# Optimization experiments

Measured on AMD Instinct MI355X. Metric: run time of the kernel, lower is better.

The kernel has to match this reference:

```python
import jax, jax.numpy as jnp
import numpy as np

NUM_NODES = 65536       # B * gcn_nodes_num = 256 * 256
NODES_PER_GRAPH = 256
GCN_EMB_DIM = 128
N_EMBD = 512
NUM_EDGES = 1048576     # avg degree 16
NEG_SLOPE = 0.1


def gcn_conv(x, edge_index, W, b, num_nodes):
    """PyG GCNConv: add self-loops, symmetric normalization, linear, aggregate."""
    loop = jnp.arange(num_nodes, dtype=edge_index.dtype)
    src = jnp.concatenate([edge_index[0], loop])
    dst = jnp.concatenate([edge_index[1], loop])
    deg = jax.ops.segment_sum(jnp.ones_like(dst, dtype=x.dtype), dst,
                              num_segments=num_nodes)
    dinv = jnp.where(deg > 0, jax.lax.rsqrt(deg), jnp.zeros_like(deg))
    norm = dinv[src] * dinv[dst]              # [E+N]
    h = x @ W                                 # [N, out]
    msg = h[src] * norm[:, None]              # [E+N, out]
    out = jax.ops.segment_sum(msg, dst, num_segments=num_nodes)
    return out + b


def setup_inputs() -> dict:
    key = jax.random.key(0)
    ks = jax.random.split(key, 8)
    nodes = jax.random.normal(ks[0], (NUM_NODES, 3), dtype=jnp.float32)
    edge_index = jax.random.randint(ks[1], (2, NUM_EDGES), 0, NUM_NODES,
                                    dtype=jnp.int64)
    W1 = jax.random.normal(ks[2], (3, 3), dtype=jnp.float32) * 0.5
    b1 = jnp.zeros((3,), dtype=jnp.float32)
    W2 = jax.random.normal(ks[3], (3, GCN_EMB_DIM), dtype=jnp.float32) * 0.5
    b2 = jnp.zeros((GCN_EMB_DIM,), dtype=jnp.float32)
    W3 = jax.random.normal(ks[4], (GCN_EMB_DIM * NODES_PER_GRAPH, N_EMBD),
                           dtype=jnp.float32) * 0.01
    b3 = jnp.zeros((N_EMBD,), dtype=jnp.float32)
    return {"nodes": nodes, "edge_index": edge_index,
            "W1": W1, "b1": b1, "W2": W2, "b2": b2, "W3": W3, "b3": b3}


def reference(nodes, edge_index, W1, b1, W2, b2, W3, b3):
    n = nodes.shape[0]
    h = gcn_conv(nodes, edge_index, W1, b1, n)           # GCNConv(3,3)
    h = jnp.where(h >= 0, h, NEG_SLOPE * h)              # leaky_relu(0.1)
    h = gcn_conv(h, edge_index, W2, b2, n)               # GCNConv(3,128)
    h = h.reshape(-1, GCN_EMB_DIM * NODES_PER_GRAPH)     # [B, 128*256]
    out = h @ W3 + b3                                    # [B, 512]
    return out
```

## Files before the change

### kernel.cpp

```cpp
#include <hip/hip_runtime.h>

static constexpr int NN   = 65536;
static constexpr int NPG  = 256;
static constexpr int NB   = 256;
static constexpr int EMB  = 128;
static constexpr int NOUT = 512;

static constexpr int NBIN = 256;
static constexpr int CAP  = 4608;

static constexpr int BT = 8;
static constexpr int KS = 16;
static constexpr int IC = NPG / KS;

__global__ __launch_bounds__(1024)
void k_partV(const int* __restrict__ src, const int* __restrict__ dst, int E,
             int* __restrict__ gbin, int* __restrict__ part,
             const float* __restrict__ W2, const float* __restrict__ b2,
             const float* __restrict__ W3, float4* __restrict__ V4) {
    union SH {
        struct { int hist[NBIN]; int loff[NBIN]; int base[NBIN]; int scanbuf[NBIN];
                 int stage[4096]; } part;
        struct { float4 red[8][4][128]; } bv;
    };
    __shared__ SH sh;
    int tid = threadIdx.x;
    int bid = blockIdx.x;

    if (bid >= NBIN) {
        int i  = bid - NBIN;
        int j4 = tid & 127;
        int cg = tid >> 7;
        const float4* w3 = (const float4*)(W3 + (size_t)i * EMB * NOUT)
                           + (size_t)cg * 16 * (NOUT/4) + j4;
        float4 a0 = {0,0,0,0}, a1 = {0,0,0,0}, a2 = {0,0,0,0}, a3 = {0,0,0,0};
        for (int c = 0; c < 16; c++) {
            float4 v = w3[(size_t)c * (NOUT/4)];
            int cc = cg*16 + c;
            float w0 = W2[0*EMB+cc], w1 = W2[1*EMB+cc], w2 = W2[2*EMB+cc], wb = b2[cc];
            a0.x += w0*v.x; a0.y += w0*v.y; a0.z += w0*v.z; a0.w += w0*v.w;
            a1.x += w1*v.x; a1.y += w1*v.y; a1.z += w1*v.z; a1.w += w1*v.w;
            a2.x += w2*v.x; a2.y += w2*v.y; a2.z += w2*v.z; a2.w += w2*v.w;
            a3.x += wb*v.x; a3.y += wb*v.y; a3.z += wb*v.z; a3.w += wb*v.w;
        }
        sh.bv.red[cg][0][j4] = a0;
        sh.bv.red[cg][1][j4] = a1;
        sh.bv.red[cg][2][j4] = a2;
        sh.bv.red[cg][3][j4] = a3;
        __syncthreads();
        if (tid < 512) {
            int k = tid >> 7, jj = tid & 127;
            float4 s = sh.bv.red[0][k][jj];
#pragma unroll
            for (int g = 1; g < 8; g++) {
                float4 v = sh.bv.red[g][k][jj];
                s.x += v.x; s.y += v.y; s.z += v.z; s.w += v.w;
            }
            sh.bv.red[0][k][jj] = s;
        }
        __syncthreads();
        if (tid < NOUT) {
            int j = tid;
            const float* r0 = (const float*)&sh.bv.red[0][0][j >> 2];
            const float* r1 = (const float*)&sh.bv.red[0][1][j >> 2];
            const float* r2 = (const float*)&sh.bv.red[0][2][j >> 2];
            const float* r3 = (const float*)&sh.bv.red[0][3][j >> 2];
            float4 o = { r0[j & 3], r1[j & 3], r2[j & 3], r3[j & 3] };
            V4[(size_t)i * NOUT + j] = o;
        }
        return;
    }
    int epb = (E + NBIN - 1) / NBIN;
    int e0 = bid * epb;
    int e1 = min(e0 + epb, E);
    if (tid < NBIN) sh.part.hist[tid] = 0;
    __syncthreads();

    int pk[4], bn[4], rk[4];
    int n = 0;
    int e = e0 + tid * 4;
    if (e + 4 <= e1) {
        int4 s4 = *(const int4*)(src + e);
        int4 d4 = *(const int4*)(dst + e);
        int ss[4] = {s4.x, s4.y, s4.z, s4.w};
        int dd[4] = {d4.x, d4.y, d4.z, d4.w};
#pragma unroll
        for (int k = 0; k < 4; k++) {
            pk[k] = ss[k] | ((dd[k] & 255) << 16);
            bn[k] = dd[k] >> 8;
            rk[k] = atomicAdd(&sh.part.hist[bn[k]], 1);
        }
        n = 4;
    } else {
        for (int k = 0; k < 4 && e + k < e1; k++) {
            int s = src[e+k], d = dst[e+k];
            pk[n] = s | ((d & 255) << 16);
            bn[n] = d >> 8;
            rk[n] = atomicAdd(&sh.part.hist[bn[n]], 1);
            n++;
        }
    }
    __syncthreads();

    if (tid < NBIN) sh.part.scanbuf[tid] = sh.part.hist[tid];
    __syncthreads();
    for (int off = 1; off < NBIN; off <<= 1) {
        int v = 0;
        if (tid < NBIN && tid >= off) v = sh.part.scanbuf[tid - off];
        __syncthreads();
        if (tid < NBIN) sh.part.scanbuf[tid] += v;
        __syncthreads();
    }
    if (tid < NBIN) {
        sh.part.loff[tid] = sh.part.scanbuf[tid] - sh.part.hist[tid];
        sh.part.base[tid] = atomicAdd(&gbin[tid], sh.part.hist[tid]);
    }
    __syncthreads();

    for (int k = 0; k < n; k++) sh.part.stage[sh.part.loff[bn[k]] + rk[k]] = pk[k];
    __syncthreads();

    int bin = tid >> 2;
    int cnt = sh.part.hist[bin], bs = sh.part.base[bin], lo = sh.part.loff[bin];
    for (int t = tid & 3; t < cnt; t += 4) {
        int gp = bs + t;
        if (gp < CAP) part[bin * CAP + gp] = sh.part.stage[lo + t];
    }
}

__global__ __launch_bounds__(512)
void k_csr(const int* __restrict__ gbin, const int* __restrict__ part,
           const float* __restrict__ nodes,
           float* __restrict__ dinv, float4* __restrict__ y1,
           int* __restrict__ rs, unsigned short* __restrict__ srt) {
    __shared__ int pkst[CAP];
    __shared__ int hist[NPG], scanb[NPG], off_[NPG];
    __shared__ unsigned short stageS[CAP];
    int tid = threadIdx.x, bin = blockIdx.x;
    if (tid < NPG) hist[tid] = 0;
    __syncthreads();
    int cnt = min(gbin[bin], CAP);
    const int* pp = part + (size_t)bin * CAP;
    for (int e = tid; e < cnt; e += 512) {
        int p = pp[e];
        pkst[e] = p;
        atomicAdd(&hist[(p >> 16) & 255], 1);
    }
    __syncthreads();
    if (tid < NPG) scanb[tid] = hist[tid];
    __syncthreads();
    for (int off = 1; off < NPG; off <<= 1) {
        int v = 0;
        if (tid < NPG && tid >= off) v = scanb[tid - off];
        __syncthreads();
        if (tid < NPG) scanb[tid] += v;
        __syncthreads();
    }
    if (tid < NPG) {
        int start = scanb[tid] - hist[tid];
        off_[tid] = start;
        int node = bin * NPG + tid;
        float di = rsqrtf((float)(hist[tid] + 1));
        dinv[node] = di;
        y1[node] = make_float4(nodes[3*node+0] * di, nodes[3*node+1] * di,
                               nodes[3*node+2] * di, 0.f);
        rs[node] = start | (hist[tid] << 20);
    }
    __syncthreads();
    for (int e = tid; e < cnt; e += 512) {
        int p = pkst[e];
        int pos = atomicAdd(&off_[(p >> 16) & 255], 1);
        stageS[pos] = (unsigned short)(p & 0xFFFF);
    }
    __syncthreads();
    const unsigned int* so = (const unsigned int*)stageS;
    unsigned int* g = (unsigned int*)(srt + (size_t)bin * CAP);
    for (int t = tid; t < (cnt + 1) >> 1; t += 512) g[t] = so[t];
}

__device__ __forceinline__ void agg_pass(int g, const int* __restrict__ rs,
                                         const unsigned short* __restrict__ srt,
                                         const float* __restrict__ dinv,
                                         const float* __restrict__ W1,
                                         const float* __restrict__ b1,
                                         const float4* __restrict__ yin,
                                         float4* __restrict__ yout, bool first) {
    int i = g >> 3, sub = g & 7;
    int rsd = rs[i];
    int start = rsd & 0xFFFFF, deg = rsd >> 20;
    const unsigned short* sp = srt + (size_t)(i >> 8) * CAP + start;
    float ax = 0.f, ay = 0.f, az = 0.f;
    for (int k = sub; k < deg; k += 8) {
        float4 v = yin[sp[k]];
        ax += v.x; ay += v.y; az += v.z;
    }
    ax += __shfl_xor(ax, 1); ay += __shfl_xor(ay, 1); az += __shfl_xor(az, 1);
    ax += __shfl_xor(ax, 2); ay += __shfl_xor(ay, 2); az += __shfl_xor(az, 2);
    ax += __shfl_xor(ax, 4); ay += __shfl_xor(ay, 4); az += __shfl_xor(az, 4);
    if (sub == 0) {
        float4 self = yin[i];
        float di = dinv[i];
        float a0 = (ax + self.x) * di, a1 = (ay + self.y) * di, a2 = (az + self.z) * di;
        if (first) {
            float h[3];
#pragma unroll
            for (int k = 0; k < 3; k++) {
                float t = a0 * W1[0*3+k] + a1 * W1[1*3+k] + a2 * W1[2*3+k] + b1[k];
                t = (t >= 0.f) ? t : 0.1f * t;
                h[k] = t * di;
            }
            yout[i] = make_float4(h[0], h[1], h[2], 0.f);
        } else {
            yout[i] = make_float4(a0, a1, a2, 0.f);
        }
    }
}

__global__ void k_agg1(const int* __restrict__ rs, const unsigned short* __restrict__ srt,
                       const float* __restrict__ dinv, const float4* __restrict__ y1,
                       const float* __restrict__ W1, const float* __restrict__ b1,
                       float4* __restrict__ y2) {
    agg_pass(blockIdx.x * 256 + threadIdx.x, rs, srt, dinv, W1, b1, y1, y2, true);
}

__global__ void k_agg2(const int* __restrict__ rs, const unsigned short* __restrict__ srt,
                       const float* __restrict__ dinv, const float4* __restrict__ y2,
                       float4* __restrict__ agg2) {
    agg_pass(blockIdx.x * 256 + threadIdx.x, rs, srt, dinv, nullptr, nullptr,
             y2, agg2, false);
}

__global__ void k_out_part(const float4* __restrict__ agg2, const float4* __restrict__ V4,
                           float* __restrict__ part) {
    __shared__ float4 a_s[BT * IC];
    int tid = threadIdx.x;
    int j  = blockIdx.x * 256 + tid;
    int b0 = blockIdx.y * BT;
    int i0 = blockIdx.z * IC;
    for (int idx = tid; idx < BT * IC; idx += 256) {
        int t = idx / IC, i = idx % IC;
        a_s[idx] = agg2[(size_t)(b0 + t) * NPG + i0 + i];
    }
    __syncthreads();

    float acc[BT];
#pragma unroll
    for (int t = 0; t < BT; t++) acc[t] = 0.f;

    const float4* vj = V4 + (size_t)i0 * NOUT + j;
    for (int i = 0; i < IC; i++) {
        float4 v = vj[(size_t)i * NOUT];
#pragma unroll
        for (int t = 0; t < BT; t++) {
            float4 a = a_s[t*IC + i];
            acc[t] += a.x * v.x + a.y * v.y + a.z * v.z + v.w;
        }
    }
#pragma unroll
    for (int t = 0; t < BT; t++)
        part[((size_t)blockIdx.z * NB + b0 + t) * NOUT + j] = acc[t];
}

__global__ void k_reduce(const float4* __restrict__ part4, const float4* __restrict__ b3_4,
                         float4* __restrict__ out4) {
    int idx = blockIdx.x * 256 + threadIdx.x;
    int j4 = idx & (NOUT/4 - 1);
    float4 acc = b3_4[j4];
#pragma unroll
    for (int s = 0; s < KS; s++) {
        float4 v = part4[(size_t)s * (NB*NOUT/4) + idx];
        acc.x += v.x; acc.y += v.y; acc.z += v.z; acc.w += v.w;
    }
    out4[idx] = acc;
}

extern "C" void kernel_launch(void* const* d_in, const int* in_sizes, int n_in,
                              void* d_out, int out_size, void* d_ws, size_t ws_size,
                              hipStream_t stream) {
    const float* nodes = (const float*)d_in[0];
    const int*   ei    = (const int*)  d_in[1];
    const float* W1    = (const float*)d_in[2];
    const float* b1    = (const float*)d_in[3];
    const float* W2    = (const float*)d_in[4];
    const float* b2    = (const float*)d_in[5];
    const float* W3    = (const float*)d_in[6];
    const float* b3    = (const float*)d_in[7];

    const int E = in_sizes[1] / 2;
    const int* src = ei;
    const int* dst = ei + E;

    char* ws = (char*)d_ws;
    int*    gbin  = (int*)ws;
    float4* y1    = (float4*)(ws + 1024);
    float4* y2    = y1 + NN;
    float4* agg2  = y2 + NN;
    float4* V4    = agg2 + NN;
    float*  partO = (float*)(V4 + (size_t)NPG * NOUT);
    int*    partE = (int*)(partO + (size_t)KS * NB * NOUT);
    unsigned short* srt = (unsigned short*)(partE + (size_t)NBIN * CAP);
    int*    rs    = (int*)(srt + (size_t)NBIN * CAP);
    float*  dinv  = (float*)(rs + NN);

    hipMemsetAsync(gbin, 0, NBIN * 4, stream);
    k_partV   <<<2*NBIN, 1024, 0, stream>>>(src, dst, E, gbin, partE, W2, b2, W3, V4);
    k_csr     <<<NBIN,    512, 0, stream>>>(gbin, partE, nodes, dinv, y1, rs, srt);
    k_agg1    <<<NN*8/256, 256, 0, stream>>>(rs, srt, dinv, y1, W1, b1, y2);
    k_agg2    <<<NN*8/256, 256, 0, stream>>>(rs, srt, dinv, y2, agg2);
    k_out_part<<<dim3(2, NB/BT, KS), 256, 0, stream>>>(agg2, V4, partO);
    k_reduce  <<<NB*NOUT/4/256,      256, 0, stream>>>((const float4*)partO,
                                                       (const float4*)b3, (float4*)d_out);
}
```

Baseline: 159.2 us.

## Spread V precompute across partition, CSR and aggregation kernels

The precompute of V (W2/b2 folded into W3, 256 rows) used to run entirely inside the partition kernel as 256 extra blocks. It is now split into four slices of 64 rows, each placed as extra blocks in the partition, CSR-build and two aggregation kernels, so the W3 streaming overlaps with latency-bound graph work in each stage. In exchange, the CSR and aggregation kernels gain larger shared-memory footprints and extra blocks, and V rows built by blocks with fewer threads use more loop iterations per block.

```diff
diff --git a/kernel.cpp b/kernel.cpp
--- a/kernel.cpp
+++ b/kernel.cpp
@@ -8,70 +8,80 @@
 
 static constexpr int NBIN = 256;
 static constexpr int CAP  = 4608;
+static constexpr int VB   = 64;
 
 static constexpr int BT = 8;
 static constexpr int KS = 16;
 static constexpr int IC = NPG / KS;
 
+template<int NCG>
+__device__ __forceinline__ void buildV_row(int i, int tid,
+        const float* __restrict__ W2, const float* __restrict__ b2,
+        const float* __restrict__ W3, float4* __restrict__ V4,
+        float4 (*red)[4][128]) {
+    constexpr int CPG = 128 / NCG;
+    constexpr int T   = NCG * 128;
+    int j4 = tid & 127;
+    int cg = tid >> 7;
+    const float4* w3 = (const float4*)(W3 + (size_t)i * EMB * NOUT)
+                       + (size_t)cg * CPG * (NOUT/4) + j4;
+    float4 a0 = {0,0,0,0}, a1 = {0,0,0,0}, a2 = {0,0,0,0}, a3 = {0,0,0,0};
+    for (int c = 0; c < CPG; c++) {
+        float4 v = w3[(size_t)c * (NOUT/4)];
+        int cc = cg * CPG + c;
+        float w0 = W2[0*EMB+cc], w1 = W2[1*EMB+cc], w2 = W2[2*EMB+cc], wb = b2[cc];
+        a0.x += w0*v.x; a0.y += w0*v.y; a0.z += w0*v.z; a0.w += w0*v.w;
+        a1.x += w1*v.x; a1.y += w1*v.y; a1.z += w1*v.z; a1.w += w1*v.w;
+        a2.x += w2*v.x; a2.y += w2*v.y; a2.z += w2*v.z; a2.w += w2*v.w;
+        a3.x += wb*v.x; a3.y += wb*v.y; a3.z += wb*v.z; a3.w += wb*v.w;
+    }
+    red[cg][0][j4] = a0;
+    red[cg][1][j4] = a1;
+    red[cg][2][j4] = a2;
+    red[cg][3][j4] = a3;
+    __syncthreads();
+    for (int idx = tid; idx < 4 * 128; idx += T) {
+        int k = idx >> 7, jj = idx & 127;
+        float4 s = red[0][k][jj];
+#pragma unroll
+        for (int g = 1; g < NCG; g++) {
+            float4 v = red[g][k][jj];
+            s.x += v.x; s.y += v.y; s.z += v.z; s.w += v.w;
+        }
+        red[0][k][jj] = s;
+    }
+    __syncthreads();
+    for (int j = tid; j < NOUT; j += T) {
+        const float* r0 = (const float*)&red[0][0][j >> 2];
+        const float* r1 = (const float*)&red[0][1][j >> 2];
+        const float* r2 = (const float*)&red[0][2][j >> 2];
+        const float* r3 = (const float*)&red[0][3][j >> 2];
+        float4 o = { r0[j & 3], r1[j & 3], r2[j & 3], r3[j & 3] };
+        V4[(size_t)i * NOUT + j] = o;
+    }
+}
+
 __global__ __launch_bounds__(1024)
-void k_partV(const int* __restrict__ src, const int* __restrict__ dst, int E,
-             int* __restrict__ gbin, int* __restrict__ part,
-             const float* __restrict__ W2, const float* __restrict__ b2,
-             const float* __restrict__ W3, float4* __restrict__ V4) {
+void k_part(const int* __restrict__ src, const int* __restrict__ dst, int E,
+            int* __restrict__ gbin, int* __restrict__ part,
+            const float* __restrict__ W2, const float* __restrict__ b2,
+            const float* __restrict__ W3, float4* __restrict__ V4) {
     union SH {
         struct { int hist[NBIN]; int loff[NBIN]; int base[NBIN]; int scanbuf[NBIN];
                  int stage[4096]; } part;
-        struct { float4 red[8][4][128]; } bv;
+        float4 red[8][4][128];
     };
     __shared__ SH sh;
     int tid = threadIdx.x;
     int bid = blockIdx.x;
 
-    if (bid >= NBIN) {
-        int i  = bid - NBIN;
-        int j4 = tid & 127;
-        int cg = tid >> 7;
-        const float4* w3 = (const float4*)(W3 + (size_t)i * EMB * NOUT)
-                           + (size_t)cg * 16 * (NOUT/4) + j4;
-        float4 a0 = {0,0,0,0}, a1 = {0,0,0,0}, a2 = {0,0,0,0}, a3 = {0,0,0,0};
-        for (int c = 0; c < 16; c++) {
-            float4 v = w3[(size_t)c * (NOUT/4)];
-            int cc = cg*16 + c;
-            float w0 = W2[0*EMB+cc], w1 = W2[1*EMB+cc], w2 = W2[2*EMB+cc], wb = b2[cc];
-            a0.x += w0*v.x; a0.y += w0*v.y; a0.z += w0*v.z; a0.w += w0*v.w;
-            a1.x += w1*v.x; a1.y += w1*v.y; a1.z += w1*v.z; a1.w += w1*v.w;
-            a2.x += w2*v.x; a2.y += w2*v.y; a2.z += w2*v.z; a2.w += w2*v.w;
-            a3.x += wb*v.x; a3.y += wb*v.y; a3.z += wb*v.z; a3.w += wb*v.w;
-        }
-        sh.bv.red[cg][0][j4] = a0;
-        sh.bv.red[cg][1][j4] = a1;
-        sh.bv.red[cg][2][j4] = a2;
-        sh.bv.red[cg][3][j4] = a3;
-        __syncthreads();
-        if (tid < 512) {
-            int k = tid >> 7, jj = tid & 127;
-            float4 s = sh.bv.red[0][k][jj];
-#pragma unroll
-            for (int g = 1; g < 8; g++) {
-                float4 v = sh.bv.red[g][k][jj];
-                s.x += v.x; s.y += v.y; s.z += v.z; s.w += v.w;
-            }
-            sh.bv.red[0][k][jj] = s;
-        }
-        __syncthreads();
-        if (tid < NOUT) {
-            int j = tid;
-            const float* r0 = (const float*)&sh.bv.red[0][0][j >> 2];
-            const float* r1 = (const float*)&sh.bv.red[0][1][j >> 2];
-            const float* r2 = (const float*)&sh.bv.red[0][2][j >> 2];
-            const float* r3 = (const float*)&sh.bv.red[0][3][j >> 2];
-            float4 o = { r0[j & 3], r1[j & 3], r2[j & 3], r3[j & 3] };
-            V4[(size_t)i * NOUT + j] = o;
-        }
+    if (bid < VB) {
+        buildV_row<8>(bid, tid, W2, b2, W3, V4, sh.red);
         return;
     }
+    int pbid = bid - VB;
     int epb = (E + NBIN - 1) / NBIN;
-    int e0 = bid * epb;
+    int e0 = pbid * epb;
     int e1 = min(e0 + epb, E);
     if (tid < NBIN) sh.part.hist[tid] = 0;
     __syncthreads();
@@ -129,51 +139,62 @@
 }
 
 __global__ __launch_bounds__(512)
-void k_csr(const int* __restrict__ gbin, const int* __restrict__ part,
-           const float* __restrict__ nodes,
-           float* __restrict__ dinv, float4* __restrict__ y1,
-           int* __restrict__ rs, unsigned short* __restrict__ srt) {
-    __shared__ int pkst[CAP];
-    __shared__ int hist[NPG], scanb[NPG], off_[NPG];
-    __shared__ unsigned short stageS[CAP];
-    int tid = threadIdx.x, bin = blockIdx.x;
-    if (tid < NPG) hist[tid] = 0;
+void k_csrV(const int* __restrict__ gbin, const int* __restrict__ part,
+            const float* __restrict__ nodes,
+            float* __restrict__ dinv, float4* __restrict__ y1,
+            int* __restrict__ rs, unsigned short* __restrict__ srt,
+            const float* __restrict__ W2, const float* __restrict__ b2,
+            const float* __restrict__ W3, float4* __restrict__ V4) {
+    union SH {
+        struct { int pkst[CAP]; int hist[NPG]; int scanb[NPG]; int off_[NPG];
+                 unsigned short stageS[CAP]; } csr;
+        float4 red[4][4][128];
+    };
+    __shared__ SH sh;
+    int tid = threadIdx.x, bid = blockIdx.x;
+
+    if (bid < VB) {
+        buildV_row<4>(VB + bid, tid, W2, b2, W3, V4, sh.red);
+        return;
+    }
+    int bin = bid - VB;
+    if (tid < NPG) sh.csr.hist[tid] = 0;
     __syncthreads();
     int cnt = min(gbin[bin], CAP);
     const int* pp = part + (size_t)bin * CAP;
     for (int e = tid; e < cnt; e += 512) {
         int p = pp[e];
-        pkst[e] = p;
-        atomicAdd(&hist[(p >> 16) & 255], 1);
-    }
-    __syncthreads();
-    if (tid < NPG) scanb[tid] = hist[tid];
+        sh.csr.pkst[e] = p;
+        atomicAdd(&sh.csr.hist[(p >> 16) & 255], 1);
+    }
+    __syncthreads();
+    if (tid < NPG) sh.csr.scanb[tid] = sh.csr.hist[tid];
     __syncthreads();
     for (int off = 1; off < NPG; off <<= 1) {
         int v = 0;
-        if (tid < NPG && tid >= off) v = scanb[tid - off];
+        if (tid < NPG && tid >= off) v = sh.csr.scanb[tid - off];
         __syncthreads();
-        if (tid < NPG) scanb[tid] += v;
+        if (tid < NPG) sh.csr.scanb[tid] += v;
         __syncthreads();
     }
     if (tid < NPG) {
-        int start = scanb[tid] - hist[tid];
-        off_[tid] = start;
+        int start = sh.csr.scanb[tid] - sh.csr.hist[tid];
+        sh.csr.off_[tid] = start;
         int node = bin * NPG + tid;
-        float di = rsqrtf((float)(hist[tid] + 1));
+        float di = rsqrtf((float)(sh.csr.hist[tid] + 1));
         dinv[node] = di;
         y1[node] = make_float4(nodes[3*node+0] * di, nodes[3*node+1] * di,
                                nodes[3*node+2] * di, 0.f);
-        rs[node] = start | (hist[tid] << 20);
+        rs[node] = start | (sh.csr.hist[tid] << 20);
     }
     __syncthreads();
     for (int e = tid; e < cnt; e += 512) {
-        int p = pkst[e];
-        int pos = atomicAdd(&off_[(p >> 16) & 255], 1);
-        stageS[pos] = (unsigned short)(p & 0xFFFF);
-    }
-    __syncthreads();
-    const unsigned int* so = (const unsigned int*)stageS;
+        int p = sh.csr.pkst[e];
+        int pos = atomicAdd(&sh.csr.off_[(p >> 16) & 255], 1);
+        sh.csr.stageS[pos] = (unsigned short)(p & 0xFFFF);
+    }
+    __syncthreads();
+    const unsigned int* so = (const unsigned int*)sh.csr.stageS;
     unsigned int* g = (unsigned int*)(srt + (size_t)bin * CAP);
     for (int t = tid; t < (cnt + 1) >> 1; t += 512) g[t] = so[t];
 }
@@ -216,17 +237,34 @@
     }
 }
 
-__global__ void k_agg1(const int* __restrict__ rs, const unsigned short* __restrict__ srt,
-                       const float* __restrict__ dinv, const float4* __restrict__ y1,
-                       const float* __restrict__ W1, const float* __restrict__ b1,
-                       float4* __restrict__ y2) {
-    agg_pass(blockIdx.x * 256 + threadIdx.x, rs, srt, dinv, W1, b1, y1, y2, true);
-}
-
-__global__ void k_agg2(const int* __restrict__ rs, const unsigned short* __restrict__ srt,
-                       const float* __restrict__ dinv, const float4* __restrict__ y2,
-                       float4* __restrict__ agg2) {
-    agg_pass(blockIdx.x * 256 + threadIdx.x, rs, srt, dinv, nullptr, nullptr,
+__global__ __launch_bounds__(256)
+void k_agg1(const int* __restrict__ rs, const unsigned short* __restrict__ srt,
+            const float* __restrict__ dinv, const float4* __restrict__ y1,
+            const float* __restrict__ W1, const float* __restrict__ b1,
+            float4* __restrict__ y2,
+            const float* __restrict__ W2, const float* __restrict__ b2,
+            const float* __restrict__ W3, float4* __restrict__ V4) {
+    __shared__ float4 red[2][4][128];
+    if (blockIdx.x < VB) {
+        buildV_row<2>(2 * VB + blockIdx.x, threadIdx.x, W2, b2, W3, V4, red);
+        return;
+    }
+    agg_pass((blockIdx.x - VB) * 256 + threadIdx.x, rs, srt, dinv, W1, b1,
+             y1, y2, true);
+}
+
+__global__ __launch_bounds__(256)
+void k_agg2(const int* __restrict__ rs, const unsigned short* __restrict__ srt,
+            const float* __restrict__ dinv, const float4* __restrict__ y2,
+            float4* __restrict__ agg2,
+            const float* __restrict__ W2, const float* __restrict__ b2,
+            const float* __restrict__ W3, float4* __restrict__ V4) {
+    __shared__ float4 red[2][4][128];
+    if (blockIdx.x < VB) {
+        buildV_row<2>(3 * VB + blockIdx.x, threadIdx.x, W2, b2, W3, V4, red);
+        return;
+    }
+    agg_pass((blockIdx.x - VB) * 256 + threadIdx.x, rs, srt, dinv, nullptr, nullptr,
              y2, agg2, false);
 }
 
@@ -303,10 +341,14 @@
     float*  dinv  = (float*)(rs + NN);
 
     hipMemsetAsync(gbin, 0, NBIN * 4, stream);
-    k_partV   <<<2*NBIN, 1024, 0, stream>>>(src, dst, E, gbin, partE, W2, b2, W3, V4);
-    k_csr     <<<NBIN,    512, 0, stream>>>(gbin, partE, nodes, dinv, y1, rs, srt);
-    k_agg1    <<<NN*8/256, 256, 0, stream>>>(rs, srt, dinv, y1, W1, b1, y2);
-    k_agg2    <<<NN*8/256, 256, 0, stream>>>(rs, srt, dinv, y2, agg2);
+    k_part    <<<VB + NBIN,      1024, 0, stream>>>(src, dst, E, gbin, partE,
+                                                    W2, b2, W3, V4);
+    k_csrV    <<<VB + NBIN,       512, 0, stream>>>(gbin, partE, nodes, dinv, y1,
+                                                    rs, srt, W2, b2, W3, V4);
+    k_agg1    <<<VB + NN*8/256,   256, 0, stream>>>(rs, srt, dinv, y1, W1, b1, y2,
+                                                    W2, b2, W3, V4);
+    k_agg2    <<<VB + NN*8/256,   256, 0, stream>>>(rs, srt, dinv, y2, agg2,
+                                                    W2, b2, W3, V4);
     k_out_part<<<dim3(2, NB/BT, KS), 256, 0, stream>>>(agg2, V4, partO);
     k_reduce  <<<NB*NOUT/4/256,      256, 0, stream>>>((const float4*)partO,
                                                        (const float4*)b3, (float4*)d_out);
```

Result: slower. 174.9 us (+9.9%).
